# Kernel tuning notes

Measured on AMD Instinct MI355X. Metric: run time of the kernel, lower is better.

Reference implementation:

```python
import jax, jax.numpy as jnp
import numpy as np

N_NODES = 50000
N_EDGES = 800000
N_GRAPHS = 64
D_IN = 128
DIMS = (256, 256)


def _glorot(key, shape):
    fan_in, fan_out = shape[0], shape[1]
    lim = jnp.sqrt(6.0 / (fan_in + fan_out)).astype(jnp.float32)
    return jax.random.uniform(key, shape, jnp.float32, -lim, lim)


def setup_inputs() -> dict:
    key = jax.random.key(0)
    ks = jax.random.split(key, 12)
    x = jax.random.normal(ks[0], (N_NODES, D_IN), dtype=jnp.float32)
    edge_index = jax.random.randint(ks[1], (2, N_EDGES), 0, N_NODES, dtype=jnp.int64)
    batch = jnp.sort(jax.random.randint(ks[2], (N_NODES,), 0, N_GRAPHS, dtype=jnp.int64))
    # MLP params per GIN layer: Linear(in,dim) -> ReLU -> Linear(dim,dim) -> ReLU
    W1_0 = _glorot(ks[3], (D_IN, DIMS[0]))
    b1_0 = jnp.zeros((DIMS[0],), jnp.float32)
    W2_0 = _glorot(ks[4], (DIMS[0], DIMS[0]))
    b2_0 = jnp.zeros((DIMS[0],), jnp.float32)
    W1_1 = _glorot(ks[5], (DIMS[0], DIMS[1]))
    b1_1 = jnp.zeros((DIMS[1],), jnp.float32)
    W2_1 = _glorot(ks[6], (DIMS[1], DIMS[1]))
    b2_1 = jnp.zeros((DIMS[1],), jnp.float32)
    return {"x": x, "edge_index": edge_index, "batch": batch,
            "W1_0": W1_0, "b1_0": b1_0, "W2_0": W2_0, "b2_0": b2_0,
            "W1_1": W1_1, "b1_1": b1_1, "W2_1": W2_1, "b2_1": b2_1}


def _gin_layer(x, src, dst, W1, b1, W2, b2):
    # aggregate: sum of neighbor features (messages from src into dst)
    agg = jax.ops.segment_sum(x[src], dst, num_segments=N_NODES)
    h = x + agg  # (1 + eps) * x + agg, eps = 0
    h = jax.nn.relu(h @ W1 + b1)
    h = jax.nn.relu(h @ W2 + b2)
    return h


def reference(x, edge_index, batch, W1_0, b1_0, W2_0, b2_0, W1_1, b1_1, W2_1, b2_1):
    src, dst = edge_index[0], edge_index[1]
    h = _gin_layer(x, src, dst, W1_0, b1_0, W2_0, b2_0)
    h = _gin_layer(h, src, dst, W1_1, b1_1, W2_1, b2_1)
    # global mean pool over graphs
    sums = jax.ops.segment_sum(h, batch, num_segments=N_GRAPHS)
    counts = jax.ops.segment_sum(jnp.ones((h.shape[0],), h.dtype), batch, num_segments=N_GRAPHS)
    return sums / jnp.maximum(counts, 1.0)[:, None]
```

## Files before the change

### kernel.cpp

```cpp
#include <hip/hip_runtime.h>


typedef __bf16 bf16x8 __attribute__((ext_vector_type(8)));
typedef float f32x4 __attribute__((ext_vector_type(4)));

#define N_NODES 50000
#define N_EDGES 800000
#define N_GRAPHS 64
#define SCAN_BLOCKS 196
#define NREP 8

#define PB_HIST0 3125
#define PB_P0    6250
#define PB_P1    6378
#define PB_P2    6634
#define PB_P3    6890
#define PB_BIAS  7146
#define PB_TOTAL 7150

#define OFF_FLAGS  0ull
#define OFF_WB     64ull
#define OFF_WP0    4096ull
#define OFF_WP1    (OFF_WP0 + 65536ull)
#define OFF_WP2    (OFF_WP1 + 131072ull)
#define OFF_WP3    (OFF_WP2 + 131072ull)
#define OFF_CNT    462848ull
#define OFF_ROWPTR 662864ull
#define OFF_CURSOR 862880ull
#define OFF_SSRC   1062912ull
#define OFF_A      2662912ull
#define OFF_B      15462912ull
#define OFF_POOL32 66662912ull
#define OFF_BSUM   67187200ull
#define OFF_PERM   67191296ull

__device__ __forceinline__ float b2f(unsigned short u) {
  union { unsigned int i; float f; } v; v.i = ((unsigned int)u) << 16; return v.f;
}
__device__ __forceinline__ float b2f_lo(unsigned int u) {
  union { unsigned int i; float f; } v; v.i = u << 16; return v.f;
}
__device__ __forceinline__ float b2f_hi(unsigned int u) {
  union { unsigned int i; float f; } v; v.i = u & 0xffff0000u; return v.f;
}
__device__ __forceinline__ unsigned short f2b(float f) {
  union { unsigned int i; float f; } v; v.f = f;
  unsigned int r = v.i + 0x7fffu + ((v.i >> 16) & 1u);
  return (unsigned short)(r >> 16);
}
__device__ __forceinline__ unsigned int pk2(float hi, float lo) {
  return ((unsigned int)f2b(hi) << 16) | f2b(lo);
}
__device__ __forceinline__ void acc8(float* a, uint4 v) {
  a[0] += b2f_lo(v.x); a[1] += b2f_hi(v.x);
  a[2] += b2f_lo(v.y); a[3] += b2f_hi(v.y);
  a[4] += b2f_lo(v.z); a[5] += b2f_hi(v.z);
  a[6] += b2f_lo(v.w); a[7] += b2f_hi(v.w);
}

__global__ void detect_zero(const unsigned int* __restrict__ xw,
                            const unsigned int* __restrict__ eiw,
                            int* __restrict__ flags,
                            int* __restrict__ counts, float* __restrict__ pool32) {
  if (blockIdx.x == 0) {
    __shared__ int s_f[256], s_i[256];
    int t = threadIdx.x;
    int fh = 0, iz = 0;
    for (int i = t; i < 1024; i += 256) {
      unsigned int e = (xw[i] >> 7) & 0xFFu;
      fh += (e >= 115u && e <= 130u) ? 1 : 0;
      iz += (eiw[2 * i + 1] == 0u) ? 1 : 0;
    }
    s_f[t] = fh; s_i[t] = iz;
    __syncthreads();
    for (int s = 128; s > 0; s >>= 1) {
      if (t < s) { s_f[t] += s_f[t + s]; s_i[t] += s_i[t + s]; }
      __syncthreads();
    }
    if (t == 0) { flags[0] = s_f[0] > 512 ? 1 : 0; flags[1] = s_i[0] > 512 ? 1 : 0; }
  } else {
    int i = (blockIdx.x - 1) * 256 + threadIdx.x;
    if (i < N_NODES) counts[i] = 0;
    if (i < NREP * N_GRAPHS * 256) pool32[i] = 0.f;
  }
}

__device__ __forceinline__ void pack_w_elem(const void* W, unsigned short* Wp,
                                            int e, int isb) {
  int n = e & 255;
  int krow = e >> 8;
  int kb = krow >> 5, r = krow & 31;
  int q = r >> 3, j = r & 7;
  size_t out = ((((size_t)(kb << 8) + n) << 2) + q) * 8 + j;
  Wp[out] = isb ? ((const unsigned short*)W)[e] : f2b(((const float*)W)[e]);
}

__global__ void prep_kernel(const void* __restrict__ x, const int* __restrict__ ei,
                            const void* W0, const void* W1, const void* W2, const void* W3,
                            const void* b0, const void* b1, const void* b2, const void* b3,
                            unsigned short* __restrict__ A,
                            int* __restrict__ counts,
                            unsigned short* __restrict__ Wp0, unsigned short* __restrict__ Wp1,
                            unsigned short* __restrict__ Wp2, unsigned short* __restrict__ Wp3,
                            unsigned short* __restrict__ Wb,
                            const int* __restrict__ flags) {
  int b = blockIdx.x, t = threadIdx.x;
  int isb = flags[0];
  if (b < PB_HIST0) {
    if (!isb) {
      int i = b * 256 + t;
      const float4* f = (const float4*)x;
      float4 a = f[2 * i], c = f[2 * i + 1];
      ushort4 o0; o0.x = f2b(a.x); o0.y = f2b(a.y); o0.z = f2b(a.z); o0.w = f2b(a.w);
      ushort4 o1; o1.x = f2b(c.x); o1.y = f2b(c.y); o1.z = f2b(c.z); o1.w = f2b(c.w);
      ((ushort4*)A)[2 * i] = o0;
      ((ushort4*)A)[2 * i + 1] = o1;
    }
  } else if (b < PB_P0) {
    int e = (b - PB_HIST0) * 256 + t;
    int dst = flags[1] ? ei[2 * (N_EDGES + e)] : ei[N_EDGES + e];
    atomicAdd(&counts[dst], 1);
  } else if (b < PB_P1) {
    pack_w_elem(W0, Wp0, (b - PB_P0) * 256 + t, isb);
  } else if (b < PB_P2) {
    pack_w_elem(W1, Wp1, (b - PB_P1) * 256 + t, isb);
  } else if (b < PB_P3) {
    pack_w_elem(W2, Wp2, (b - PB_P2) * 256 + t, isb);
  } else if (b < PB_BIAS) {
    pack_w_elem(W3, Wp3, (b - PB_P3) * 256 + t, isb);
  } else {
    int i = (b - PB_BIAS) * 256 + t;
    const void* p = (i < 256) ? b0 : (i < 512) ? b1 : (i < 768) ? b2 : b3;
    int n = i & 255;
    Wb[i] = isb ? ((const unsigned short*)p)[n] : f2b(((const float*)p)[n]);
  }
}

__global__ void scan_blocks(const int* __restrict__ counts,
                            int* __restrict__ rowptr, int* __restrict__ bsum) {
  __shared__ int sd[256];
  int t = threadIdx.x;
  int i = blockIdx.x * 256 + t;
  int v = (i < N_NODES) ? counts[i] : 0;
  sd[t] = v;
  __syncthreads();
  for (int off = 1; off < 256; off <<= 1) {
    int u = (t >= off) ? sd[t - off] : 0;
    __syncthreads();
    sd[t] += u;
    __syncthreads();
  }
  if (i < N_NODES) rowptr[i] = sd[t] - v;
  if (t == 255) bsum[blockIdx.x] = sd[255];
}

__global__ void scan_fix(int* __restrict__ rowptr, int* __restrict__ cursor,
                         const int* __restrict__ bsum, const int* __restrict__ counts,
                         int* __restrict__ perm) {
  __shared__ int sb[256], lh[256], lc2[256];
  int t = threadIdx.x;
  sb[t] = (t < SCAN_BLOCKS) ? bsum[t] : 0;
  lh[t] = 0; lc2[t] = 0;
  __syncthreads();
  for (int off = 1; off < 256; off <<= 1) {
    int u = (t >= off) ? sb[t - off] : 0;
    __syncthreads();
    sb[t] += u;
    __syncthreads();
  }
  int boffv = (blockIdx.x > 0) ? sb[blockIdx.x - 1] : 0;
  int i = blockIdx.x * 256 + t;
  int d = 0;
  int valid = (i < N_NODES);
  if (valid) {
    int v = rowptr[i] + boffv;
    rowptr[i] = v;
    cursor[i] = v;
    int c = counts[i];
    d = c > 255 ? 255 : c;
    atomicAdd(&lh[d], 1);
  }
  if (i == 0) rowptr[N_NODES] = N_EDGES;
  __syncthreads();
  int own = lh[t];
  for (int off = 1; off < 256; off <<= 1) {
    int u = (t >= off) ? lh[t - off] : 0;
    __syncthreads();
    lh[t] += u;
    __syncthreads();
  }
  int ex = lh[t] - own;
  __syncthreads();
  lh[t] = ex;
  __syncthreads();
  if (valid) {
    int r = lh[d] + atomicAdd(&lc2[d], 1);
    perm[blockIdx.x * 256 + r] = i;
  }
}

__global__ void fill_kernel(const int* __restrict__ ei, int* __restrict__ cursor,
                            unsigned short* __restrict__ ssrc,
                            const int* __restrict__ flags) {
  int e = blockIdx.x * blockDim.x + threadIdx.x;
  if (e >= N_EDGES) return;
  int is64 = flags[1];
  int src = is64 ? ei[2 * e] : ei[e];
  int dst = is64 ? ei[2 * (N_EDGES + e)] : ei[N_EDGES + e];
  int pos = atomicAdd(&cursor[dst], 1);
  ssrc[pos] = (unsigned short)src;
}

__global__ void __launch_bounds__(256) fused_layer1(
    const unsigned short* __restrict__ featCanon,
    const unsigned short* __restrict__ featRaw,
    const int* __restrict__ rowptr, const unsigned short* __restrict__ ssrc,
    const int* __restrict__ perm,
    const unsigned short* __restrict__ Wp0, const unsigned short* __restrict__ Wp1,
    const unsigned short* __restrict__ Wb,
    unsigned short* __restrict__ B, const int* __restrict__ flags) {
  __shared__ __align__(16) unsigned short Alds[16 * 136];
  __shared__ __align__(16) unsigned short Tlds[16 * 264];
  __shared__ int sp[16];
  const int row0 = blockIdx.x << 4;
  const int lane = threadIdx.x & 63;
  const int wave = threadIdx.x >> 6;
  const unsigned short* feat = flags[0] ? featRaw : featCanon;
  if (threadIdx.x < 16) sp[threadIdx.x] = perm[row0 + threadIdx.x];
  __syncthreads();

  {
    int sub = lane >> 4, l = lane & 15;
    int nl = (wave << 2) + sub;
    int node = sp[nl];
    int beg = rowptr[node], end = rowptr[node + 1];
    int deg = end - beg;
    int c = l << 3;
    float a[8];
#pragma unroll
    for (int j = 0; j < 8; ++j) a[j] = 0.f;
    acc8(a, *(const uint4*)(feat + (size_t)node * 128 + c));
    int pre0 = (l < deg) ? (int)ssrc[beg + l] : 0;
    int pre1 = (16 + l < deg) ? (int)ssrc[beg + 16 + l] : 0;
    int lim = deg < 32 ? deg : 32;
    int i = 0;
    for (; i + 3 < lim; i += 4) {
      uint4 v[4];
#pragma unroll
      for (int e = 0; e < 4; ++e) {
        int ee = i + e;
        int idx = __shfl(ee < 16 ? pre0 : pre1, ee & 15, 16);
        v[e] = *(const uint4*)(feat + (size_t)idx * 128 + c);
      }
#pragma unroll
      for (int e = 0; e < 4; ++e) acc8(a, v[e]);
    }
    for (; i < lim; ++i) {
      int idx = __shfl(i < 16 ? pre0 : pre1, i & 15, 16);
      acc8(a, *(const uint4*)(feat + (size_t)idx * 128 + c));
    }
    for (; i < deg; ++i)
      acc8(a, *(const uint4*)(feat + (size_t)ssrc[beg + i] * 128 + c));
    uint4 o;
    o.x = pk2(a[1], a[0]); o.y = pk2(a[3], a[2]);
    o.z = pk2(a[5], a[4]); o.w = pk2(a[7], a[6]);
    *(uint4*)(&Alds[nl * 136 + c]) = o;
  }
  __syncthreads();

  const int m = lane & 15, q = lane >> 4;
  {
    f32x4 acc[4];
#pragma unroll
    for (int t = 0; t < 4; ++t) acc[t] = (f32x4){0.f, 0.f, 0.f, 0.f};
    const unsigned short* arow = &Alds[m * 136 + (q << 3)];
    const int nb = (wave << 6) + m;
#pragma unroll
    for (int kb = 0; kb < 4; ++kb) {
      bf16x8 af = *(const bf16x8*)(arow + (kb << 5));
      const unsigned short* wp = Wp0 + (((size_t)(kb << 8) + nb) * 4 + q) * 8;
      acc[0] = __builtin_amdgcn_mfma_f32_16x16x32_bf16(af, *(const bf16x8*)(wp), acc[0], 0, 0, 0);
      acc[1] = __builtin_amdgcn_mfma_f32_16x16x32_bf16(af, *(const bf16x8*)(wp + 512), acc[1], 0, 0, 0);
      acc[2] = __builtin_amdgcn_mfma_f32_16x16x32_bf16(af, *(const bf16x8*)(wp + 1024), acc[2], 0, 0, 0);
      acc[3] = __builtin_amdgcn_mfma_f32_16x16x32_bf16(af, *(const bf16x8*)(wp + 1536), acc[3], 0, 0, 0);
    }
#pragma unroll
    for (int t = 0; t < 4; ++t) {
      int n = (wave << 6) + (t << 4) + m;
      float bv = b2f(Wb[n]);
#pragma unroll
      for (int i = 0; i < 4; ++i)
        Tlds[((q << 2) + i) * 264 + n] = f2b(fmaxf(acc[t][i] + bv, 0.f));
    }
  }
  __syncthreads();

  {
    f32x4 acc[4];
#pragma unroll
    for (int t = 0; t < 4; ++t) acc[t] = (f32x4){0.f, 0.f, 0.f, 0.f};
    const unsigned short* arow = &Tlds[m * 264 + (q << 3)];
    const int nb = (wave << 6) + m;
#pragma unroll
    for (int kb = 0; kb < 8; ++kb) {
      bf16x8 af = *(const bf16x8*)(arow + (kb << 5));
      const unsigned short* wp = Wp1 + (((size_t)(kb << 8) + nb) * 4 + q) * 8;
      acc[0] = __builtin_amdgcn_mfma_f32_16x16x32_bf16(af, *(const bf16x8*)(wp), acc[0], 0, 0, 0);
      acc[1] = __builtin_amdgcn_mfma_f32_16x16x32_bf16(af, *(const bf16x8*)(wp + 512), acc[1], 0, 0, 0);
      acc[2] = __builtin_amdgcn_mfma_f32_16x16x32_bf16(af, *(const bf16x8*)(wp + 1024), acc[2], 0, 0, 0);
      acc[3] = __builtin_amdgcn_mfma_f32_16x16x32_bf16(af, *(const bf16x8*)(wp + 1536), acc[3], 0, 0, 0);
    }
#pragma unroll
    for (int t = 0; t < 4; ++t) {
      int n = (wave << 6) + (t << 4) + m;
      float bv = b2f(Wb[256 + n]);
#pragma unroll
      for (int i = 0; i < 4; ++i) {
        int r = sp[(q << 2) + i];
        B[(size_t)r * 256 + n] = f2b(fmaxf(acc[t][i] + bv, 0.f));
      }
    }
  }
}

__global__ void __launch_bounds__(512) fused_layer2(
    const unsigned short* __restrict__ B,
    const int* __restrict__ rowptr, const unsigned short* __restrict__ ssrc,
    const int* __restrict__ perm,
    const unsigned short* __restrict__ Wp2, const unsigned short* __restrict__ Wp3,
    const unsigned short* __restrict__ Wb,
    float* __restrict__ pool32, const int* __restrict__ batch,
    const int* __restrict__ flags) {
  __shared__ __align__(16) unsigned short Alds[16 * 264];
  __shared__ __align__(16) unsigned short Tlds[16 * 264];
  __shared__ int sp[16], sg[16], uni;
  const int row0 = blockIdx.x << 4;
  const int lane = threadIdx.x & 63;
  const int wave = threadIdx.x >> 6;
  if (threadIdx.x < 16) {
    int p = perm[row0 + threadIdx.x];
    sp[threadIdx.x] = p;
    sg[threadIdx.x] = flags[1] ? batch[2 * p] : batch[p];
  }
  __syncthreads();
  if (threadIdx.x == 0) {
    int u = 1;
#pragma unroll
    for (int i = 1; i < 16; ++i) u &= (sg[i] == sg[0]);
    uni = u;
  }

  {
    int sub = lane >> 5, l = lane & 31;
    int nl = (wave << 1) + sub;
    int node = sp[nl];
    int beg = rowptr[node], end = rowptr[node + 1];
    int deg = end - beg;
    int c = l << 3;
    float a[8];
#pragma unroll
    for (int j = 0; j < 8; ++j) a[j] = 0.f;
    acc8(a, *(const uint4*)(B + (size_t)node * 256 + c));
    int pre0 = (l < deg) ? (int)ssrc[beg + l] : 0;
    int pre1 = (32 + l < deg) ? (int)ssrc[beg + 32 + l] : 0;
    int lim = deg < 64 ? deg : 64;
    int i = 0;
    for (; i + 3 < lim; i += 4) {
      uint4 v[4];
#pragma unroll
      for (int e = 0; e < 4; ++e) {
        int ee = i + e;
        int idx = __shfl(ee < 32 ? pre0 : pre1, ee & 31, 32);
        v[e] = *(const uint4*)(B + (size_t)idx * 256 + c);
      }
#pragma unroll
      for (int e = 0; e < 4; ++e) acc8(a, v[e]);
    }
    for (; i < lim; ++i) {
      int idx = __shfl(i < 32 ? pre0 : pre1, i & 31, 32);
      acc8(a, *(const uint4*)(B + (size_t)idx * 256 + c));
    }
    for (; i < deg; ++i)
      acc8(a, *(const uint4*)(B + (size_t)ssrc[beg + i] * 256 + c));
    uint4 o;
    o.x = pk2(a[1], a[0]); o.y = pk2(a[3], a[2]);
    o.z = pk2(a[5], a[4]); o.w = pk2(a[7], a[6]);
    *(uint4*)(&Alds[nl * 264 + c]) = o;
  }
  __syncthreads();

  const int m = lane & 15, q = lane >> 4;
  {
    f32x4 acc[2];
    acc[0] = (f32x4){0.f, 0.f, 0.f, 0.f};
    acc[1] = (f32x4){0.f, 0.f, 0.f, 0.f};
    const unsigned short* arow = &Alds[m * 264 + (q << 3)];
    const int nb = (wave << 5) + m;
#pragma unroll
    for (int kb = 0; kb < 8; ++kb) {
      bf16x8 af = *(const bf16x8*)(arow + (kb << 5));
      const unsigned short* wp = Wp2 + (((size_t)(kb << 8) + nb) * 4 + q) * 8;
      acc[0] = __builtin_amdgcn_mfma_f32_16x16x32_bf16(af, *(const bf16x8*)(wp), acc[0], 0, 0, 0);
      acc[1] = __builtin_amdgcn_mfma_f32_16x16x32_bf16(af, *(const bf16x8*)(wp + 512), acc[1], 0, 0, 0);
    }
#pragma unroll
    for (int t = 0; t < 2; ++t) {
      int n = (wave << 5) + (t << 4) + m;
      float bv = b2f(Wb[512 + n]);
#pragma unroll
      for (int i = 0; i < 4; ++i)
        Tlds[((q << 2) + i) * 264 + n] = f2b(fmaxf(acc[t][i] + bv, 0.f));
    }
  }
  __syncthreads();

  {
    f32x4 acc[2];
    acc[0] = (f32x4){0.f, 0.f, 0.f, 0.f};
    acc[1] = (f32x4){0.f, 0.f, 0.f, 0.f};
    const unsigned short* arow = &Tlds[m * 264 + (q << 3)];
    const int nb = (wave << 5) + m;
#pragma unroll
    for (int kb = 0; kb < 8; ++kb) {
      bf16x8 af = *(const bf16x8*)(arow + (kb << 5));
      const unsigned short* wp = Wp3 + (((size_t)(kb << 8) + nb) * 4 + q) * 8;
      acc[0] = __builtin_amdgcn_mfma_f32_16x16x32_bf16(af, *(const bf16x8*)(wp), acc[0], 0, 0, 0);
      acc[1] = __builtin_amdgcn_mfma_f32_16x16x32_bf16(af, *(const bf16x8*)(wp + 512), acc[1], 0, 0, 0);
    }
    float* pr = pool32 + ((blockIdx.x & (NREP - 1)) << 14);
    int u = uni;
#pragma unroll
    for (int t = 0; t < 2; ++t) {
      int n = (wave << 5) + (t << 4) + m;
      float bv = b2f(Wb[768 + n]);
      float v0 = fmaxf(acc[t][0] + bv, 0.f);
      float v1 = fmaxf(acc[t][1] + bv, 0.f);
      float v2 = fmaxf(acc[t][2] + bv, 0.f);
      float v3 = fmaxf(acc[t][3] + bv, 0.f);
      if (u) {
        float ps = v0 + v1 + v2 + v3;
        ps += __shfl_xor(ps, 16);
        ps += __shfl_xor(ps, 32);
        if (q == 0) unsafeAtomicAdd(&pr[sg[0] * 256 + n], ps);
      } else {
        float vv[4] = {v0, v1, v2, v3};
        int gp = sg[q << 2];
        float a = 0.f;
#pragma unroll
        for (int i = 0; i < 4; ++i) {
          int g = sg[(q << 2) + i];
          if (g != gp) { unsafeAtomicAdd(&pr[gp * 256 + n], a); a = 0.f; gp = g; }
          a += vv[i];
        }
        unsafeAtomicAdd(&pr[gp * 256 + n], a);
      }
    }
  }
}

__device__ __forceinline__ int lower_bound(const int* a, int n, int v, int is64) {
  int lo = 0, hi = n;
  while (lo < hi) {
    int mid = (lo + hi) >> 1;
    int bv = is64 ? a[2 * mid] : a[mid];
    if (bv < v) lo = mid + 1; else hi = mid;
  }
  return lo;
}

__global__ void pool_final(const float* __restrict__ pool32,
                           const int* __restrict__ batch,
                           void* __restrict__ out,
                           const int* __restrict__ flags) {
  __shared__ int sh[2];
  int g = blockIdx.x;
  int is64 = flags[1];
  if (threadIdx.x == 0) sh[0] = lower_bound(batch, N_NODES, g, is64);
  if (threadIdx.x == 1) sh[1] = lower_bound(batch, N_NODES, g + 1, is64);
  __syncthreads();
  int c = threadIdx.x;
  float s = 0.f;
#pragma unroll
  for (int r = 0; r < NREP; ++r) s += pool32[(r << 14) + g * 256 + c];
  float res = s / fmaxf((float)(sh[1] - sh[0]), 1.0f);
  if (flags[0]) ((unsigned short*)out)[(size_t)g * 256 + c] = f2b(res);
  else          ((float*)out)[(size_t)g * 256 + c] = res;
}

extern "C" void kernel_launch(void* const* d_in, const int* in_sizes, int n_in,
                              void* d_out, int out_size, void* d_ws, size_t ws_size,
                              hipStream_t stream) {
  const void* x    = d_in[0];
  const int*  ei   = (const int*)d_in[1];
  const int*  batch= (const int*)d_in[2];

  char* ws = (char*)d_ws;
  int*            flags = (int*)(ws + OFF_FLAGS);
  unsigned short* Wb    = (unsigned short*)(ws + OFF_WB);
  unsigned short* Wp0   = (unsigned short*)(ws + OFF_WP0);
  unsigned short* Wp1   = (unsigned short*)(ws + OFF_WP1);
  unsigned short* Wp2   = (unsigned short*)(ws + OFF_WP2);
  unsigned short* Wp3   = (unsigned short*)(ws + OFF_WP3);
  int*            cnts  = (int*)(ws + OFF_CNT);
  int*            rowp  = (int*)(ws + OFF_ROWPTR);
  int*            curs  = (int*)(ws + OFF_CURSOR);
  unsigned short* ssrc  = (unsigned short*)(ws + OFF_SSRC);
  unsigned short* A     = (unsigned short*)(ws + OFF_A);
  unsigned short* B     = (unsigned short*)(ws + OFF_B);
  float*          pool32= (float*)(ws + OFF_POOL32);
  int*            bsum  = (int*)(ws + OFF_BSUM);
  int*            perm  = (int*)(ws + OFF_PERM);

  detect_zero<<<513, 256, 0, stream>>>((const unsigned int*)x, (const unsigned int*)ei,
                                       flags, cnts, pool32);
  prep_kernel<<<PB_TOTAL, 256, 0, stream>>>(x, ei,
                                            d_in[3], d_in[5], d_in[7], d_in[9],
                                            d_in[4], d_in[6], d_in[8], d_in[10],
                                            A, cnts, Wp0, Wp1, Wp2, Wp3, Wb, flags);
  scan_blocks<<<SCAN_BLOCKS, 256, 0, stream>>>(cnts, rowp, bsum);
  scan_fix<<<SCAN_BLOCKS, 256, 0, stream>>>(rowp, curs, bsum, cnts, perm);
  fill_kernel<<<3125, 256, 0, stream>>>(ei, curs, ssrc, flags);

  fused_layer1<<<3125, 256, 0, stream>>>(A, (const unsigned short*)x, rowp, ssrc,
                                         perm, Wp0, Wp1, Wb, B, flags);
  fused_layer2<<<3125, 512, 0, stream>>>(B, rowp, ssrc, perm, Wp2, Wp3, Wb,
                                         pool32, batch, flags);

  pool_final<<<N_GRAPHS, 256, 0, stream>>>(pool32, batch, d_out, flags);
}
```

Baseline: 339.2 us.

## Merge graph-build preprocessing kernels into one cooperative kernel with grid syncs

Replaces five preprocessing launches (flag detection/zeroing, prep, two scan phases, CSR fill) with a single cooperative kernel of 960 blocks that separates the phases with grid.sync(). The goal is to remove per-launch overhead and inter-kernel gaps in the setup phase. In exchange, work runs in grid-stride loops with fewer resident threads, the CSR fill and histogram phases may get less parallelism, and grid-wide barriers add their own cost.

After: 774.9 us. 128% more time.

```diff
diff --git a/kernel.cpp b/kernel.cpp
--- a/kernel.cpp
+++ b/kernel.cpp
@@ -1,4 +1,7 @@
 #include <hip/hip_runtime.h>
+#include <hip/hip_cooperative_groups.h>
+
+namespace cg = cooperative_groups;
 
 
 typedef __bf16 bf16x8 __attribute__((ext_vector_type(8)));
@@ -9,14 +12,16 @@
 #define N_GRAPHS 64
 #define SCAN_BLOCKS 196
 #define NREP 8
-
-#define PB_HIST0 3125
-#define PB_P0    6250
-#define PB_P1    6378
-#define PB_P2    6634
-#define PB_P3    6890
-#define PB_BIAS  7146
-#define PB_TOTAL 7150
+#define BUILD_BLOCKS 960
+
+#define U_CONV0 0
+#define U_HIST0 800000
+#define U_P0    1600000
+#define U_P1    1632768
+#define U_P2    1698304
+#define U_P3    1763840
+#define U_BIAS  1829376
+#define U_TOTAL 1830400
 
 #define OFF_FLAGS  0ull
 #define OFF_WB     64ull
@@ -57,34 +62,6 @@
   a[4] += b2f_lo(v.z); a[5] += b2f_hi(v.z);
   a[6] += b2f_lo(v.w); a[7] += b2f_hi(v.w);
 }
-
-__global__ void detect_zero(const unsigned int* __restrict__ xw,
-                            const unsigned int* __restrict__ eiw,
-                            int* __restrict__ flags,
-                            int* __restrict__ counts, float* __restrict__ pool32) {
-  if (blockIdx.x == 0) {
-    __shared__ int s_f[256], s_i[256];
-    int t = threadIdx.x;
-    int fh = 0, iz = 0;
-    for (int i = t; i < 1024; i += 256) {
-      unsigned int e = (xw[i] >> 7) & 0xFFu;
-      fh += (e >= 115u && e <= 130u) ? 1 : 0;
-      iz += (eiw[2 * i + 1] == 0u) ? 1 : 0;
-    }
-    s_f[t] = fh; s_i[t] = iz;
-    __syncthreads();
-    for (int s = 128; s > 0; s >>= 1) {
-      if (t < s) { s_f[t] += s_f[t + s]; s_i[t] += s_i[t + s]; }
-      __syncthreads();
-    }
-    if (t == 0) { flags[0] = s_f[0] > 512 ? 1 : 0; flags[1] = s_i[0] > 512 ? 1 : 0; }
-  } else {
-    int i = (blockIdx.x - 1) * 256 + threadIdx.x;
-    if (i < N_NODES) counts[i] = 0;
-    if (i < NREP * N_GRAPHS * 256) pool32[i] = 0.f;
-  }
-}
-
 __device__ __forceinline__ void pack_w_elem(const void* W, unsigned short* Wp,
                                             int e, int isb) {
   int n = e & 255;
@@ -95,120 +72,150 @@
   Wp[out] = isb ? ((const unsigned short*)W)[e] : f2b(((const float*)W)[e]);
 }
 
-__global__ void prep_kernel(const void* __restrict__ x, const int* __restrict__ ei,
-                            const void* W0, const void* W1, const void* W2, const void* W3,
-                            const void* b0, const void* b1, const void* b2, const void* b3,
-                            unsigned short* __restrict__ A,
-                            int* __restrict__ counts,
-                            unsigned short* __restrict__ Wp0, unsigned short* __restrict__ Wp1,
-                            unsigned short* __restrict__ Wp2, unsigned short* __restrict__ Wp3,
-                            unsigned short* __restrict__ Wb,
-                            const int* __restrict__ flags) {
-  int b = blockIdx.x, t = threadIdx.x;
-  int isb = flags[0];
-  if (b < PB_HIST0) {
-    if (!isb) {
-      int i = b * 256 + t;
-      const float4* f = (const float4*)x;
-      float4 a = f[2 * i], c = f[2 * i + 1];
-      ushort4 o0; o0.x = f2b(a.x); o0.y = f2b(a.y); o0.z = f2b(a.z); o0.w = f2b(a.w);
-      ushort4 o1; o1.x = f2b(c.x); o1.y = f2b(c.y); o1.z = f2b(c.z); o1.w = f2b(c.w);
-      ((ushort4*)A)[2 * i] = o0;
-      ((ushort4*)A)[2 * i + 1] = o1;
-    }
-  } else if (b < PB_P0) {
-    int e = (b - PB_HIST0) * 256 + t;
-    int dst = flags[1] ? ei[2 * (N_EDGES + e)] : ei[N_EDGES + e];
-    atomicAdd(&counts[dst], 1);
-  } else if (b < PB_P1) {
-    pack_w_elem(W0, Wp0, (b - PB_P0) * 256 + t, isb);
-  } else if (b < PB_P2) {
-    pack_w_elem(W1, Wp1, (b - PB_P1) * 256 + t, isb);
-  } else if (b < PB_P3) {
-    pack_w_elem(W2, Wp2, (b - PB_P2) * 256 + t, isb);
-  } else if (b < PB_BIAS) {
-    pack_w_elem(W3, Wp3, (b - PB_P3) * 256 + t, isb);
-  } else {
-    int i = (b - PB_BIAS) * 256 + t;
-    const void* p = (i < 256) ? b0 : (i < 512) ? b1 : (i < 768) ? b2 : b3;
-    int n = i & 255;
-    Wb[i] = isb ? ((const unsigned short*)p)[n] : f2b(((const float*)p)[n]);
-  }
-}
-
-__global__ void scan_blocks(const int* __restrict__ counts,
-                            int* __restrict__ rowptr, int* __restrict__ bsum) {
-  __shared__ int sd[256];
-  int t = threadIdx.x;
-  int i = blockIdx.x * 256 + t;
-  int v = (i < N_NODES) ? counts[i] : 0;
-  sd[t] = v;
-  __syncthreads();
-  for (int off = 1; off < 256; off <<= 1) {
-    int u = (t >= off) ? sd[t - off] : 0;
+__global__ void __launch_bounds__(256) build_kernel(
+    const void* __restrict__ x, const int* __restrict__ ei,
+    const void* W0, const void* W1, const void* W2, const void* W3,
+    const void* b0, const void* b1, const void* b2, const void* b3,
+    char* __restrict__ ws) {
+  cg::grid_group grid = cg::this_grid();
+  int*            flags  = (int*)(ws + OFF_FLAGS);
+  unsigned short* Wb     = (unsigned short*)(ws + OFF_WB);
+  unsigned short* Wp0    = (unsigned short*)(ws + OFF_WP0);
+  unsigned short* Wp1    = (unsigned short*)(ws + OFF_WP1);
+  unsigned short* Wp2    = (unsigned short*)(ws + OFF_WP2);
+  unsigned short* Wp3    = (unsigned short*)(ws + OFF_WP3);
+  int*            counts = (int*)(ws + OFF_CNT);
+  int*            rowptr = (int*)(ws + OFF_ROWPTR);
+  int*            cursor = (int*)(ws + OFF_CURSOR);
+  unsigned short* ssrc   = (unsigned short*)(ws + OFF_SSRC);
+  unsigned short* A      = (unsigned short*)(ws + OFF_A);
+  float*          pool32 = (float*)(ws + OFF_POOL32);
+  int*            bsum   = (int*)(ws + OFF_BSUM);
+  int*            perm   = (int*)(ws + OFF_PERM);
+
+  __shared__ int sA[256], sB[256], sC[256];
+  const int t = threadIdx.x;
+  const int gtid = blockIdx.x * 256 + t;
+  const int gs = gridDim.x * 256;
+
+  if (blockIdx.x == 0) {
+    const unsigned int* xw = (const unsigned int*)x;
+    const unsigned int* eiw = (const unsigned int*)ei;
+    int fh = 0, iz = 0;
+    for (int i = t; i < 1024; i += 256) {
+      unsigned int e = (xw[i] >> 7) & 0xFFu;
+      fh += (e >= 115u && e <= 130u) ? 1 : 0;
+      iz += (eiw[2 * i + 1] == 0u) ? 1 : 0;
+    }
+    sA[t] = fh; sB[t] = iz;
     __syncthreads();
-    sd[t] += u;
+    for (int s = 128; s > 0; s >>= 1) {
+      if (t < s) { sA[t] += sA[t + s]; sB[t] += sB[t + s]; }
+      __syncthreads();
+    }
+    if (t == 0) { flags[0] = sA[0] > 512 ? 1 : 0; flags[1] = sB[0] > 512 ? 1 : 0; }
+  }
+  for (int i = gtid; i < NREP * N_GRAPHS * 256; i += gs) pool32[i] = 0.f;
+  for (int i = gtid; i < N_NODES; i += gs) counts[i] = 0;
+  grid.sync();
+
+  const int isb = flags[0], i64 = flags[1];
+  for (int u = gtid; u < U_TOTAL; u += gs) {
+    if (u < U_HIST0) {
+      if (!isb) {
+        int i = u;
+        const float4* f = (const float4*)x;
+        float4 a = f[2 * i], c = f[2 * i + 1];
+        ushort4 o0; o0.x = f2b(a.x); o0.y = f2b(a.y); o0.z = f2b(a.z); o0.w = f2b(a.w);
+        ushort4 o1; o1.x = f2b(c.x); o1.y = f2b(c.y); o1.z = f2b(c.z); o1.w = f2b(c.w);
+        ((ushort4*)A)[2 * i] = o0;
+        ((ushort4*)A)[2 * i + 1] = o1;
+      }
+    } else if (u < U_P0) {
+      int e = u - U_HIST0;
+      int dst = i64 ? ei[2 * (N_EDGES + e)] : ei[N_EDGES + e];
+      atomicAdd(&counts[dst], 1);
+    } else if (u < U_P1) {
+      pack_w_elem(W0, Wp0, u - U_P0, isb);
+    } else if (u < U_P2) {
+      pack_w_elem(W1, Wp1, u - U_P1, isb);
+    } else if (u < U_P3) {
+      pack_w_elem(W2, Wp2, u - U_P2, isb);
+    } else if (u < U_BIAS) {
+      pack_w_elem(W3, Wp3, u - U_P3, isb);
+    } else {
+      int i = u - U_BIAS;
+      const void* p = (i < 256) ? b0 : (i < 512) ? b1 : (i < 768) ? b2 : b3;
+      int n = i & 255;
+      Wb[i] = isb ? ((const unsigned short*)p)[n] : f2b(((const float*)p)[n]);
+    }
+  }
+  grid.sync();
+
+  if (blockIdx.x < SCAN_BLOCKS) {
+    int i = blockIdx.x * 256 + t;
+    int v = (i < N_NODES) ? counts[i] : 0;
+    sA[t] = v;
     __syncthreads();
-  }
-  if (i < N_NODES) rowptr[i] = sd[t] - v;
-  if (t == 255) bsum[blockIdx.x] = sd[255];
-}
-
-__global__ void scan_fix(int* __restrict__ rowptr, int* __restrict__ cursor,
-                         const int* __restrict__ bsum, const int* __restrict__ counts,
-                         int* __restrict__ perm) {
-  __shared__ int sb[256], lh[256], lc2[256];
-  int t = threadIdx.x;
-  sb[t] = (t < SCAN_BLOCKS) ? bsum[t] : 0;
-  lh[t] = 0; lc2[t] = 0;
-  __syncthreads();
-  for (int off = 1; off < 256; off <<= 1) {
-    int u = (t >= off) ? sb[t - off] : 0;
+    for (int off = 1; off < 256; off <<= 1) {
+      int u = (t >= off) ? sA[t - off] : 0;
+      __syncthreads();
+      sA[t] += u;
+      __syncthreads();
+    }
+    if (i < N_NODES) rowptr[i] = sA[t] - v;
+    if (t == 255) bsum[blockIdx.x] = sA[255];
+  }
+  grid.sync();
+
+  if (blockIdx.x < SCAN_BLOCKS) {
+    sA[t] = (t < SCAN_BLOCKS) ? bsum[t] : 0;
+    sB[t] = 0; sC[t] = 0;
     __syncthreads();
-    sb[t] += u;
+    for (int off = 1; off < 256; off <<= 1) {
+      int u = (t >= off) ? sA[t - off] : 0;
+      __syncthreads();
+      sA[t] += u;
+      __syncthreads();
+    }
+    int boffv = (blockIdx.x > 0) ? sA[blockIdx.x - 1] : 0;
+    int i = blockIdx.x * 256 + t;
+    int d = 0;
+    int valid = (i < N_NODES);
+    if (valid) {
+      int v = rowptr[i] + boffv;
+      rowptr[i] = v;
+      cursor[i] = v;
+      int c = counts[i];
+      d = c > 255 ? 255 : c;
+      atomicAdd(&sB[d], 1);
+    }
+    if (i == 0) rowptr[N_NODES] = N_EDGES;
     __syncthreads();
-  }
-  int boffv = (blockIdx.x > 0) ? sb[blockIdx.x - 1] : 0;
-  int i = blockIdx.x * 256 + t;
-  int d = 0;
-  int valid = (i < N_NODES);
-  if (valid) {
-    int v = rowptr[i] + boffv;
-    rowptr[i] = v;
-    cursor[i] = v;
-    int c = counts[i];
-    d = c > 255 ? 255 : c;
-    atomicAdd(&lh[d], 1);
-  }
-  if (i == 0) rowptr[N_NODES] = N_EDGES;
-  __syncthreads();
-  int own = lh[t];
-  for (int off = 1; off < 256; off <<= 1) {
-    int u = (t >= off) ? lh[t - off] : 0;
+    int own = sB[t];
+    for (int off = 1; off < 256; off <<= 1) {
+      int u = (t >= off) ? sB[t - off] : 0;
+      __syncthreads();
+      sB[t] += u;
+      __syncthreads();
+    }
+    int ex = sB[t] - own;
     __syncthreads();
-    lh[t] += u;
+    sB[t] = ex;
     __syncthreads();
-  }
-  int ex = lh[t] - own;
-  __syncthreads();
-  lh[t] = ex;
-  __syncthreads();
-  if (valid) {
-    int r = lh[d] + atomicAdd(&lc2[d], 1);
-    perm[blockIdx.x * 256 + r] = i;
-  }
-}
-
-__global__ void fill_kernel(const int* __restrict__ ei, int* __restrict__ cursor,
-                            unsigned short* __restrict__ ssrc,
-                            const int* __restrict__ flags) {
-  int e = blockIdx.x * blockDim.x + threadIdx.x;
-  if (e >= N_EDGES) return;
-  int is64 = flags[1];
-  int src = is64 ? ei[2 * e] : ei[e];
-  int dst = is64 ? ei[2 * (N_EDGES + e)] : ei[N_EDGES + e];
-  int pos = atomicAdd(&cursor[dst], 1);
-  ssrc[pos] = (unsigned short)src;
+    if (valid) {
+      int r = sB[d] + atomicAdd(&sC[d], 1);
+      perm[blockIdx.x * 256 + r] = i;
+    }
+  }
+  grid.sync();
+
+  for (int e = gtid; e < N_EDGES; e += gs) {
+    int src = i64 ? ei[2 * e] : ei[e];
+    int dst = i64 ? ei[2 * (N_EDGES + e)] : ei[N_EDGES + e];
+    int pos = atomicAdd(&cursor[dst], 1);
+    ssrc[pos] = (unsigned short)src;
+  }
 }
 
 __global__ void __launch_bounds__(256) fused_layer1(
@@ -493,6 +500,14 @@
   const void* x    = d_in[0];
   const int*  ei   = (const int*)d_in[1];
   const int*  batch= (const int*)d_in[2];
+  const void* W0 = d_in[3];
+  const void* bb0 = d_in[4];
+  const void* W1 = d_in[5];
+  const void* bb1 = d_in[6];
+  const void* W2 = d_in[7];
+  const void* bb2 = d_in[8];
+  const void* W3 = d_in[9];
+  const void* bb3 = d_in[10];
 
   char* ws = (char*)d_ws;
   int*            flags = (int*)(ws + OFF_FLAGS);
@@ -501,25 +516,19 @@
   unsigned short* Wp1   = (unsigned short*)(ws + OFF_WP1);
   unsigned short* Wp2   = (unsigned short*)(ws + OFF_WP2);
   unsigned short* Wp3   = (unsigned short*)(ws + OFF_WP3);
-  int*            cnts  = (int*)(ws + OFF_CNT);
   int*            rowp  = (int*)(ws + OFF_ROWPTR);
-  int*            curs  = (int*)(ws + OFF_CURSOR);
   unsigned short* ssrc  = (unsigned short*)(ws + OFF_SSRC);
   unsigned short* A     = (unsigned short*)(ws + OFF_A);
   unsigned short* B     = (unsigned short*)(ws + OFF_B);
   float*          pool32= (float*)(ws + OFF_POOL32);
-  int*            bsum  = (int*)(ws + OFF_BSUM);
   int*            perm  = (int*)(ws + OFF_PERM);
 
-  detect_zero<<<513, 256, 0, stream>>>((const unsigned int*)x, (const unsigned int*)ei,
-                                       flags, cnts, pool32);
-  prep_kernel<<<PB_TOTAL, 256, 0, stream>>>(x, ei,
-                                            d_in[3], d_in[5], d_in[7], d_in[9],
-                                            d_in[4], d_in[6], d_in[8], d_in[10],
-                                            A, cnts, Wp0, Wp1, Wp2, Wp3, Wb, flags);
-  scan_blocks<<<SCAN_BLOCKS, 256, 0, stream>>>(cnts, rowp, bsum);
-  scan_fix<<<SCAN_BLOCKS, 256, 0, stream>>>(rowp, curs, bsum, cnts, perm);
-  fill_kernel<<<3125, 256, 0, stream>>>(ei, curs, ssrc, flags);
+  void* kargs[] = { (void*)&x, (void*)&ei,
+                    (void*)&W0, (void*)&W1, (void*)&W2, (void*)&W3,
+                    (void*)&bb0, (void*)&bb1, (void*)&bb2, (void*)&bb3,
+                    (void*)&ws };
+  hipLaunchCooperativeKernel((const void*)build_kernel,
+                             dim3(BUILD_BLOCKS), dim3(256), kargs, 0, stream);
 
   fused_layer1<<<3125, 256, 0, stream>>>(A, (const unsigned short*)x, rowp, ssrc,
                                          perm, Wp0, Wp1, Wb, B, flags);
```
